# Kernel tuning notes

Hardware: AMD Instinct MI355X
Metric: run time of the kernel (lower is better)

## Reference

```python
import jax, jax.numpy as jnp
import numpy as np

N_PED = 131072      # total pedestrians (batch)
SEG = 64            # pedestrians per segment (equal-size groups)
N_SEQ = N_PED // SEG
D_IN = 256          # enc_h_dim
D_OUT = 128         # mlp_dim


def setup_inputs() -> dict:
    key = jax.random.key(0)
    k1, k2 = jax.random.split(key, 2)
    h_states = jax.random.normal(k1, (N_PED, D_IN), dtype=jnp.float32)
    W = jax.random.normal(k2, (D_IN, D_OUT), dtype=jnp.float32) * 0.05
    b = jnp.zeros((D_OUT,), dtype=jnp.float32)
    starts = jnp.arange(N_SEQ, dtype=jnp.int64) * SEG
    seq_start_end = jnp.stack([starts, starts + SEG], axis=1)  # [N_SEQ, 2]
    return {"h_states": h_states, "W": W, "b": b, "seq_start_end": seq_start_end}


def reference(h_states, W, b, seq_start_end):
    # fc projection: (N, D_IN) -> (N, D_OUT)
    h = h_states @ W + b
    # gather each segment: equal-size groups of SEG pedestrians
    starts = seq_start_end[:, 0]                     # [G]
    idx = starts[:, None] + jnp.arange(SEG)[None, :]  # [G, S]
    seg = h[idx]                                      # [G, S, D_OUT]
    # per-segment self-attention pooling: softmax(H H^T) @ H
    scores = jnp.einsum('gsd,gtd->gst', seg, seg)     # [G, S, S]
    attn = jax.nn.softmax(scores, axis=-1)
    ctx = jnp.einsum('gst,gtd->gsd', attn, seg)       # [G, S, D_OUT]
    return ctx.reshape(-1, D_OUT)                     # [N, D_OUT]
```

## Files before the change

### kernel.cpp

```cpp
#include <hip/hip_runtime.h>
#include <stdint.h>

#define SEG 64
#define D_IN 256
#define D_OUT 128
#define NSEQ 2048

typedef __attribute__((ext_vector_type(8))) _Float16 half8;
typedef __attribute__((ext_vector_type(4))) float floatx4;

static __device__ __forceinline__ unsigned short f2h_bits(float f) {
  union { _Float16 h; unsigned short u; } v; v.h = (_Float16)f; return v.u;
}
static __device__ __forceinline__ unsigned pack2(float a, float b) {
  return (unsigned)f2h_bits(a) | ((unsigned)f2h_bits(b) << 16);
}

__global__ void prep_w_kernel(const float* __restrict__ W,
                              unsigned short* __restrict__ Wf) {
  const int idx = blockIdx.x * 256 + threadIdx.x;
  const float v = W[idx];
  const int k = idx >> 7, n = idx & 127;
  const int slot = (((n >> 4) * 8 + (k >> 5)) * 64 + ((n & 15) + 16 * ((k >> 3) & 3))) * 8 + (k & 7);
  Wf[slot] = f2h_bits(v);
}

struct SharedHT {
  unsigned short h[4][4][64][8];
  unsigned short ht[8][2][64][8];
};
union alignas(16) SharedU {
  unsigned short a[4][8][64][8];
  SharedHT s;
};

__global__ __launch_bounds__(256, 4)
void attn_fused(const float* __restrict__ hs,
                const unsigned short* __restrict__ Wf,
                const float* __restrict__ bias,
                float* __restrict__ out)
{
  __shared__ SharedU u;
  __shared__ unsigned short pbuf[4][2][64][8];

  const int g    = blockIdx.x;
  const int tid  = (int)threadIdx.x;
  const int w    = tid >> 6;
  const int lane = tid & 63;
  const int c    = lane & 15;
  const int q    = lane >> 4;

  {
    const float4* gsrc = (const float4*)(hs + (size_t)g * (SEG * D_IN));
#pragma unroll
    for (int i = 0; i < 4; ++i) {
      const int qb = i * 1024 + tid * 4;
      const float4 v0 = gsrc[qb + 0];
      const float4 v1 = gsrc[qb + 1];
      const float4 v2 = gsrc[qb + 2];
      const float4 v3 = gsrc[qb + 3];
      const int row  = i * 16 + (tid >> 4);
      const int ks   = (tid & 15) >> 1;
      const int slot = (row & 15) + ((tid & 1) << 5);
      unsigned short* d0 = &u.a[row >> 4][ks][slot][0];
      uint4 wa, wb;
      wa.x = pack2(v0.x, v0.y); wa.y = pack2(v0.z, v0.w);
      wa.z = pack2(v1.x, v1.y); wa.w = pack2(v1.z, v1.w);
      wb.x = pack2(v2.x, v2.y); wb.y = pack2(v2.z, v2.w);
      wb.z = pack2(v3.x, v3.y); wb.w = pack2(v3.z, v3.w);
      *(uint4*)d0         = wa;
      *(uint4*)(d0 + 128) = wb;
    }
  }

  const half8* WfV = (const half8*)Wf;
  const half8 wpre0 = WfV[((2 * w + 0) * 8 + 0) * 64 + lane];
  const half8 wpre1 = WfV[((2 * w + 1) * 8 + 0) * 64 + lane];

  float bv[2];
#pragma unroll
  for (int nt = 0; nt < 2; ++nt) bv[nt] = bias[(2 * w + nt) * 16 + c];
  floatx4 acc[2][4];
#pragma unroll
  for (int nt = 0; nt < 2; ++nt)
#pragma unroll
    for (int mt = 0; mt < 4; ++mt)
      acc[nt][mt] = (floatx4){bv[nt], bv[nt], bv[nt], bv[nt]};

  __syncthreads();

#pragma unroll
  for (int ks = 0; ks < 8; ++ks) {
    const half8 wf0 = ks ? WfV[((2 * w + 0) * 8 + ks) * 64 + lane] : wpre0;
    const half8 wf1 = ks ? WfV[((2 * w + 1) * 8 + ks) * 64 + lane] : wpre1;
    half8 af[4];
#pragma unroll
    for (int mt = 0; mt < 4; ++mt)
      af[mt] = *(const half8*)(&u.a[mt][ks][lane][0]);
#pragma unroll
    for (int mt = 0; mt < 4; ++mt) {
      acc[0][mt] = __builtin_amdgcn_mfma_f32_16x16x32_f16(af[mt], wf0, acc[0][mt], 0, 0, 0);
      acc[1][mt] = __builtin_amdgcn_mfma_f32_16x16x32_f16(af[mt], wf1, acc[1][mt], 0, 0, 0);
    }
  }

  __syncthreads();

#pragma unroll
  for (int nt = 0; nt < 2; ++nt) {
    const int ntg = 2 * w + nt;
#pragma unroll
    for (int mt = 0; mt < 4; ++mt) {
      unsigned short hb[4];
#pragma unroll
      for (int i = 0; i < 4; ++i) hb[i] = f2h_bits(acc[nt][mt][i]);
      const int lph = 16 * ((2 * nt + (c >> 3)) & 3);
#pragma unroll
      for (int i = 0; i < 4; ++i)
        u.s.h[mt][w][4 * q + i + lph][c & 7] = hb[i];
      const int lanep = c + 16 * ((2 * mt + (q >> 1)) & 3);
      const unsigned lo = (unsigned)hb[0] | ((unsigned)hb[1] << 16);
      const unsigned hi = (unsigned)hb[2] | ((unsigned)hb[3] << 16);
      *(uint2*)(&u.s.ht[ntg][mt >> 1][lanep][(q & 1) * 4]) = make_uint2(lo, hi);
    }
  }

  __syncthreads();

  floatx4 sacc[4];
#pragma unroll
  for (int nt = 0; nt < 4; ++nt) sacc[nt] = (floatx4){0.f, 0.f, 0.f, 0.f};
#pragma unroll
  for (int ks = 0; ks < 4; ++ks) {
    const half8 a = *(const half8*)(&u.s.h[w][ks][lane][0]);
#pragma unroll
    for (int nt = 0; nt < 4; ++nt) {
      const half8 b = *(const half8*)(&u.s.h[nt][ks][lane][0]);
      sacc[nt] = __builtin_amdgcn_mfma_f32_16x16x32_f16(a, b, sacc[nt], 0, 0, 0);
    }
  }

  float ev[4][4];
  float inv[4];
#pragma unroll
  for (int i = 0; i < 4; ++i) {
    float m = fmaxf(fmaxf(sacc[0][i], sacc[1][i]), fmaxf(sacc[2][i], sacc[3][i]));
#pragma unroll
    for (int d = 1; d < 16; d <<= 1) m = fmaxf(m, __shfl_xor(m, d, 64));
    float ssum = 0.f;
#pragma unroll
    for (int nt = 0; nt < 4; ++nt) {
      ev[i][nt] = __expf(sacc[nt][i] - m);
      ssum += ev[i][nt];
    }
#pragma unroll
    for (int d = 1; d < 16; d <<= 1) ssum += __shfl_xor(ssum, d, 64);
    inv[i] = 1.0f / ssum;
  }

#pragma unroll
  for (int i = 0; i < 4; ++i)
#pragma unroll
    for (int nt = 0; nt < 4; ++nt)
      pbuf[w][nt >> 1][4 * q + i + 16 * ((2 * nt + (c >> 3)) & 3)][c & 7] =
          f2h_bits(ev[i][nt] * inv[i]);

  floatx4 cacc[8];
#pragma unroll
  for (int nt = 0; nt < 8; ++nt) cacc[nt] = (floatx4){0.f, 0.f, 0.f, 0.f};
#pragma unroll
  for (int kt = 0; kt < 2; ++kt) {
    const half8 a = *(const half8*)(&pbuf[w][kt][lane][0]);
#pragma unroll
    for (int nt = 0; nt < 8; ++nt) {
      const half8 b = *(const half8*)(&u.s.ht[nt][kt][lane][0]);
      cacc[nt] = __builtin_amdgcn_mfma_f32_16x16x32_f16(a, b, cacc[nt], 0, 0, 0);
    }
  }

  float* ob = out + (size_t)g * (SEG * D_OUT) + (size_t)(16 * w + 4 * q) * D_OUT + c;
#pragma unroll
  for (int i = 0; i < 4; ++i)
#pragma unroll
    for (int nt = 0; nt < 8; ++nt)
      ob[i * D_OUT + 16 * nt] = cacc[nt][i];
}

extern "C" void kernel_launch(void* const* d_in, const int* in_sizes, int n_in,
                              void* d_out, int out_size, void* d_ws, size_t ws_size,
                              hipStream_t stream) {
  const float* hs   = (const float*)d_in[0];
  const float* W    = (const float*)d_in[1];
  const float* bias = (const float*)d_in[2];
  float* out = (float*)d_out;
  unsigned short* Wf = (unsigned short*)d_ws;

  prep_w_kernel<<<128, 256, 0, stream>>>(W, Wf);
  attn_fused<<<NSEQ, 256, 0, stream>>>(hs, Wf, bias, out);
}
```

Baseline: 220.8 us.

## Load A fragments directly from global, per-wave row tiles, vectorized transposed output

The projection GEMM now has each wave own 16 rows and all 8 output column tiles. It loads its A fragments straight from global memory and converts them to fp16 in registers, which removes the LDS staging of h_states and one barrier. The final PV matmul swaps operands so each lane holds 4 consecutive output columns, allowing 16-byte vector stores instead of scalar strided stores. In exchange, every wave now reads the full W fragment set from global/L2 (8 tiles instead of 2), and the global A loads are strided per lane rather than fully coalesced.

```diff
diff --git a/kernel.cpp b/kernel.cpp
--- a/kernel.cpp
+++ b/kernel.cpp
@@ -25,13 +25,9 @@
   Wf[slot] = f2h_bits(v);
 }
 
-struct SharedHT {
+struct SharedFrag {
   unsigned short h[4][4][64][8];
   unsigned short ht[8][2][64][8];
-};
-union alignas(16) SharedU {
-  unsigned short a[4][8][64][8];
-  SharedHT s;
 };
 
 __global__ __launch_bounds__(256, 4)
@@ -40,7 +36,7 @@
                 const float* __restrict__ bias,
                 float* __restrict__ out)
 {
-  __shared__ SharedU u;
+  __shared__ SharedFrag u;
   __shared__ unsigned short pbuf[4][2][64][8];
 
   const int g    = blockIdx.x;
@@ -50,79 +46,43 @@
   const int c    = lane & 15;
   const int q    = lane >> 4;
 
-  {
-    const float4* gsrc = (const float4*)(hs + (size_t)g * (SEG * D_IN));
+  floatx4 acc[8];
 #pragma unroll
-    for (int i = 0; i < 4; ++i) {
-      const int qb = i * 1024 + tid * 4;
-      const float4 v0 = gsrc[qb + 0];
-      const float4 v1 = gsrc[qb + 1];
-      const float4 v2 = gsrc[qb + 2];
-      const float4 v3 = gsrc[qb + 3];
-      const int row  = i * 16 + (tid >> 4);
-      const int ks   = (tid & 15) >> 1;
-      const int slot = (row & 15) + ((tid & 1) << 5);
-      unsigned short* d0 = &u.a[row >> 4][ks][slot][0];
-      uint4 wa, wb;
-      wa.x = pack2(v0.x, v0.y); wa.y = pack2(v0.z, v0.w);
-      wa.z = pack2(v1.x, v1.y); wa.w = pack2(v1.z, v1.w);
-      wb.x = pack2(v2.x, v2.y); wb.y = pack2(v2.z, v2.w);
-      wb.z = pack2(v3.x, v3.y); wb.w = pack2(v3.z, v3.w);
-      *(uint4*)d0         = wa;
-      *(uint4*)(d0 + 128) = wb;
+  for (int nt = 0; nt < 8; ++nt) {
+    const float bv = bias[16 * nt + c];
+    acc[nt] = (floatx4){bv, bv, bv, bv};
+  }
+
+  const float* arow = hs + ((size_t)g * SEG + 16 * w + c) * D_IN + 8 * q;
+  const half8* WfV = (const half8*)Wf;
+#pragma unroll
+  for (int ks = 0; ks < 8; ++ks) {
+    const float4 a0 = *(const float4*)(arow + 32 * ks);
+    const float4 a1 = *(const float4*)(arow + 32 * ks + 4);
+    union { uint4 u4; half8 h8; } cv;
+    cv.u4.x = pack2(a0.x, a0.y); cv.u4.y = pack2(a0.z, a0.w);
+    cv.u4.z = pack2(a1.x, a1.y); cv.u4.w = pack2(a1.z, a1.w);
+    const half8 af = cv.h8;
+#pragma unroll
+    for (int nt = 0; nt < 8; ++nt) {
+      const half8 wfv = WfV[(nt * 8 + ks) * 64 + lane];
+      acc[nt] = __builtin_amdgcn_mfma_f32_16x16x32_f16(af, wfv, acc[nt], 0, 0, 0);
     }
   }
 
-  const half8* WfV = (const half8*)Wf;
-  const half8 wpre0 = WfV[((2 * w + 0) * 8 + 0) * 64 + lane];
-  const half8 wpre1 = WfV[((2 * w + 1) * 8 + 0) * 64 + lane];
-
-  float bv[2];
 #pragma unroll
-  for (int nt = 0; nt < 2; ++nt) bv[nt] = bias[(2 * w + nt) * 16 + c];
-  floatx4 acc[2][4];
+  for (int nt = 0; nt < 8; ++nt) {
+    unsigned short hb[4];
 #pragma unroll
-  for (int nt = 0; nt < 2; ++nt)
+    for (int i = 0; i < 4; ++i) hb[i] = f2h_bits(acc[nt][i]);
+    const int lph = 16 * ((2 * nt + (c >> 3)) & 3);
 #pragma unroll
-    for (int mt = 0; mt < 4; ++mt)
-      acc[nt][mt] = (floatx4){bv[nt], bv[nt], bv[nt], bv[nt]};
-
-  __syncthreads();
-
-#pragma unroll
-  for (int ks = 0; ks < 8; ++ks) {
-    const half8 wf0 = ks ? WfV[((2 * w + 0) * 8 + ks) * 64 + lane] : wpre0;
-    const half8 wf1 = ks ? WfV[((2 * w + 1) * 8 + ks) * 64 + lane] : wpre1;
-    half8 af[4];
-#pragma unroll
-    for (int mt = 0; mt < 4; ++mt)
-      af[mt] = *(const half8*)(&u.a[mt][ks][lane][0]);
-#pragma unroll
-    for (int mt = 0; mt < 4; ++mt) {
-      acc[0][mt] = __builtin_amdgcn_mfma_f32_16x16x32_f16(af[mt], wf0, acc[0][mt], 0, 0, 0);
-      acc[1][mt] = __builtin_amdgcn_mfma_f32_16x16x32_f16(af[mt], wf1, acc[1][mt], 0, 0, 0);
-    }
-  }
-
-  __syncthreads();
-
-#pragma unroll
-  for (int nt = 0; nt < 2; ++nt) {
-    const int ntg = 2 * w + nt;
-#pragma unroll
-    for (int mt = 0; mt < 4; ++mt) {
-      unsigned short hb[4];
-#pragma unroll
-      for (int i = 0; i < 4; ++i) hb[i] = f2h_bits(acc[nt][mt][i]);
-      const int lph = 16 * ((2 * nt + (c >> 3)) & 3);
-#pragma unroll
-      for (int i = 0; i < 4; ++i)
-        u.s.h[mt][w][4 * q + i + lph][c & 7] = hb[i];
-      const int lanep = c + 16 * ((2 * mt + (q >> 1)) & 3);
-      const unsigned lo = (unsigned)hb[0] | ((unsigned)hb[1] << 16);
-      const unsigned hi = (unsigned)hb[2] | ((unsigned)hb[3] << 16);
-      *(uint2*)(&u.s.ht[ntg][mt >> 1][lanep][(q & 1) * 4]) = make_uint2(lo, hi);
-    }
+    for (int i = 0; i < 4; ++i)
+      u.h[w][nt >> 1][4 * q + i + lph][c & 7] = hb[i];
+    const unsigned lo = (unsigned)hb[0] | ((unsigned)hb[1] << 16);
+    const unsigned hi = (unsigned)hb[2] | ((unsigned)hb[3] << 16);
+    *(uint2*)&u.ht[nt][w >> 1][c + 16 * ((2 * w + (q >> 1)) & 3)][4 * (q & 1)] =
+        make_uint2(lo, hi);
   }
 
   __syncthreads();
@@ -132,10 +92,10 @@
   for (int nt = 0; nt < 4; ++nt) sacc[nt] = (floatx4){0.f, 0.f, 0.f, 0.f};
 #pragma unroll
   for (int ks = 0; ks < 4; ++ks) {
-    const half8 a = *(const half8*)(&u.s.h[w][ks][lane][0]);
+    const half8 a = *(const half8*)(&u.h[w][ks][lane][0]);
 #pragma unroll
     for (int nt = 0; nt < 4; ++nt) {
-      const half8 b = *(const half8*)(&u.s.h[nt][ks][lane][0]);
+      const half8 b = *(const half8*)(&u.h[nt][ks][lane][0]);
       sacc[nt] = __builtin_amdgcn_mfma_f32_16x16x32_f16(a, b, sacc[nt], 0, 0, 0);
     }
   }
@@ -167,23 +127,21 @@
 
   floatx4 cacc[8];
 #pragma unroll
-  for (int nt = 0; nt < 8; ++nt) cacc[nt] = (floatx4){0.f, 0.f, 0.f, 0.f};
+  for (int dt = 0; dt < 8; ++dt) cacc[dt] = (floatx4){0.f, 0.f, 0.f, 0.f};
 #pragma unroll
   for (int kt = 0; kt < 2; ++kt) {
-    const half8 a = *(const half8*)(&pbuf[w][kt][lane][0]);
+    const half8 pf = *(const half8*)(&pbuf[w][kt][lane][0]);
 #pragma unroll
-    for (int nt = 0; nt < 8; ++nt) {
-      const half8 b = *(const half8*)(&u.s.ht[nt][kt][lane][0]);
-      cacc[nt] = __builtin_amdgcn_mfma_f32_16x16x32_f16(a, b, cacc[nt], 0, 0, 0);
+    for (int dt = 0; dt < 8; ++dt) {
+      const half8 hf = *(const half8*)(&u.ht[dt][kt][lane][0]);
+      cacc[dt] = __builtin_amdgcn_mfma_f32_16x16x32_f16(hf, pf, cacc[dt], 0, 0, 0);
     }
   }
 
-  float* ob = out + (size_t)g * (SEG * D_OUT) + (size_t)(16 * w + 4 * q) * D_OUT + c;
+  float* orow = out + ((size_t)g * SEG + 16 * w + c) * D_OUT + 4 * q;
 #pragma unroll
-  for (int i = 0; i < 4; ++i)
-#pragma unroll
-    for (int nt = 0; nt < 8; ++nt)
-      ob[i * D_OUT + 16 * nt] = cacc[nt][i];
+  for (int dt = 0; dt < 8; ++dt)
+    *(floatx4*)(orow + 16 * dt) = cacc[dt];
 }
 
 extern "C" void kernel_launch(void* const* d_in, const int* in_sizes, int n_in,
```

After: 230.7 us. 1.05x slower.
